# Kernel optimization log

Measured on AMD Instinct MI355X. Metric: run time of the kernel, lower is better.

## Reference

```python
import jax, jax.numpy as jnp
import numpy as np

S, B, C, H, W = 4, 8, 9, 512, 512

def setup_inputs() -> dict:
    key = jax.random.key(0)
    k1, k2 = jax.random.split(key)
    predictions = jax.random.normal(k1, (S, B, C, H, W), dtype=jnp.float32)
    w = jax.random.normal(k2, (S, C), dtype=jnp.float32) * 0.1  # 1x1 conv weights per stage
    b = jnp.zeros((S,), dtype=jnp.float32)                      # 1x1 conv biases per stage
    return {"predictions": predictions, "w": w, "b": b}

def reference(predictions, w, b):
    # per-stage 1x1 conv (C -> 1): [S,B,H,W]
    wm = jnp.einsum('sbchw,sc->sbhw', predictions, w) + b[:, None, None, None]
    # softmax over stage dim S
    weights = jax.nn.softmax(wm, axis=0)  # [S,B,H,W]
    # weighted sum over stages -> [B,C,H,W]
    fused = jnp.einsum('sbhw,sbchw->bchw', weights, predictions)
    return fused
```

## Files before the change

kernel.cpp:

```cpp
#include <hip/hip_runtime.h>
#include <math.h>

constexpr int  Sn = 4;
constexpr int  Bn = 8;
constexpr int  Cn = 9;
constexpr int  HWc = 512 * 512;
constexpr long SSTRIDE = (long)Bn * Cn * HWc;

typedef float v2f __attribute__((ext_vector_type(2)));

__global__ __launch_bounds__(256) void weighted_fusion_kernel(
    const float* __restrict__ pred,
    const float* __restrict__ wmat,
    const float* __restrict__ bvec,
    float* __restrict__ out)
{
    int tid = blockIdx.x * 256 + threadIdx.x;
    long p2 = (long)tid * 2;
    int b  = (int)(p2 >> 18);
    int hw = (int)(p2 & (HWc - 1));

    const float* tbase = pred + (long)b * Cn * HWc + hw;

    v2f pr[Sn][Cn];
    #pragma unroll
    for (int s = 0; s < Sn; ++s) {
        #pragma unroll
        for (int c = 0; c < Cn; ++c) {
            const v2f* p = reinterpret_cast<const v2f*>(
                tbase + (long)s * SSTRIDE + (long)c * HWc);
            pr[s][c] = __builtin_nontemporal_load(p);
        }
    }

    v2f wm[Sn];
    #pragma unroll
    for (int s = 0; s < Sn; ++s) {
        v2f a = bvec[s];
        #pragma unroll
        for (int c = 0; c < Cn; ++c) {
            float wc = wmat[s * Cn + c];
            a += pr[s][c] * wc;
        }
        wm[s] = a;
    }

    v2f m = wm[0];
    #pragma unroll
    for (int s = 1; s < Sn; ++s) {
        m.x = fmaxf(m.x, wm[s].x);
        m.y = fmaxf(m.y, wm[s].y);
    }
    v2f p[Sn];
    v2f l = 0.0f;
    #pragma unroll
    for (int s = 0; s < Sn; ++s) {
        p[s].x = __expf(wm[s].x - m.x);
        p[s].y = __expf(wm[s].y - m.y);
        l += p[s];
    }
    v2f rl;
    rl.x = 1.0f / l.x;
    rl.y = 1.0f / l.y;
    #pragma unroll
    for (int s = 0; s < Sn; ++s) p[s] *= rl;

    float* obase = out + (long)b * Cn * HWc + hw;
    #pragma unroll
    for (int c = 0; c < Cn; ++c) {
        v2f o = p[0] * pr[0][c];
        #pragma unroll
        for (int s = 1; s < Sn; ++s) o += p[s] * pr[s][c];
        __builtin_nontemporal_store(o, reinterpret_cast<v2f*>(obase + (long)c * HWc));
    }
}

extern "C" void kernel_launch(void* const* d_in, const int* in_sizes, int n_in,
                              void* d_out, int out_size, void* d_ws, size_t ws_size,
                              hipStream_t stream) {
    const float* pred = (const float*)d_in[0];
    const float* w    = (const float*)d_in[1];
    const float* bias = (const float*)d_in[2];
    float* out        = (float*)d_out;

    const int total_threads = (Bn * HWc) / 2;
    const int block = 256;
    const int grid  = total_threads / block;
    weighted_fusion_kernel<<<grid, block, 0, stream>>>(pred, w, bias, out);
}
```

Measured before the change: 392.9 us.

## Use float4 per thread with streaming online softmax accumulation across stages

```diff
diff --git a/kernel.cpp b/kernel.cpp
--- a/kernel.cpp
+++ b/kernel.cpp
@@ -7,7 +7,7 @@
 constexpr int  HWc = 512 * 512;
 constexpr long SSTRIDE = (long)Bn * Cn * HWc;
 
-typedef float v2f __attribute__((ext_vector_type(2)));
+typedef float v4f __attribute__((ext_vector_type(4)));
 
 __global__ __launch_bounds__(256) void weighted_fusion_kernel(
     const float* __restrict__ pred,
@@ -16,62 +16,49 @@
     float* __restrict__ out)
 {
     int tid = blockIdx.x * 256 + threadIdx.x;
-    long p2 = (long)tid * 2;
-    int b  = (int)(p2 >> 18);
-    int hw = (int)(p2 & (HWc - 1));
+    long p4 = (long)tid * 4;
+    int b  = (int)(p4 >> 18);
+    int hw = (int)(p4 & (HWc - 1));
+    long toff = (long)b * Cn * HWc + hw;
 
-    const float* tbase = pred + (long)b * Cn * HWc + hw;
+    v4f acc[Cn];
+    #pragma unroll
+    for (int c = 0; c < Cn; ++c) acc[c] = 0.0f;
+    v4f l = 0.0f;
 
-    v2f pr[Sn][Cn];
     #pragma unroll
     for (int s = 0; s < Sn; ++s) {
+        v4f pr[Cn];
         #pragma unroll
         for (int c = 0; c < Cn; ++c) {
-            const v2f* p = reinterpret_cast<const v2f*>(
-                tbase + (long)s * SSTRIDE + (long)c * HWc);
-            pr[s][c] = __builtin_nontemporal_load(p);
+            const v4f* p = reinterpret_cast<const v4f*>(
+                pred + (long)s * SSTRIDE + (long)c * HWc + toff);
+            pr[c] = __builtin_nontemporal_load(p);
         }
+
+        v4f a = bvec[s];
+        #pragma unroll
+        for (int c = 0; c < Cn; ++c) a += pr[c] * wmat[s * Cn + c];
+
+        v4f e;
+        e.x = __expf(a.x); e.y = __expf(a.y);
+        e.z = __expf(a.z); e.w = __expf(a.w);
+        l += e;
+        #pragma unroll
+        for (int c = 0; c < Cn; ++c) acc[c] += pr[c] * e;
     }
 
-    v2f wm[Sn];
-    #pragma unroll
-    for (int s = 0; s < Sn; ++s) {
-        v2f a = bvec[s];
-        #pragma unroll
-        for (int c = 0; c < Cn; ++c) {
-            float wc = wmat[s * Cn + c];
-            a += pr[s][c] * wc;
-        }
-        wm[s] = a;
-    }
+    v4f rl;
+    rl.x = __builtin_amdgcn_rcpf(l.x);
+    rl.y = __builtin_amdgcn_rcpf(l.y);
+    rl.z = __builtin_amdgcn_rcpf(l.z);
+    rl.w = __builtin_amdgcn_rcpf(l.w);
 
-    v2f m = wm[0];
-    #pragma unroll
-    for (int s = 1; s < Sn; ++s) {
-        m.x = fmaxf(m.x, wm[s].x);
-        m.y = fmaxf(m.y, wm[s].y);
-    }
-    v2f p[Sn];
-    v2f l = 0.0f;
-    #pragma unroll
-    for (int s = 0; s < Sn; ++s) {
-        p[s].x = __expf(wm[s].x - m.x);
-        p[s].y = __expf(wm[s].y - m.y);
-        l += p[s];
-    }
-    v2f rl;
-    rl.x = 1.0f / l.x;
-    rl.y = 1.0f / l.y;
-    #pragma unroll
-    for (int s = 0; s < Sn; ++s) p[s] *= rl;
-
-    float* obase = out + (long)b * Cn * HWc + hw;
+    float* obase = out + toff;
     #pragma unroll
     for (int c = 0; c < Cn; ++c) {
-        v2f o = p[0] * pr[0][c];
-        #pragma unroll
-        for (int s = 1; s < Sn; ++s) o += p[s] * pr[s][c];
-        __builtin_nontemporal_store(o, reinterpret_cast<v2f*>(obase + (long)c * HWc));
+        __builtin_nontemporal_store(acc[c] * rl,
+            reinterpret_cast<v4f*>(obase + (long)c * HWc));
     }
 }
 
@@ -83,7 +70,7 @@
     const float* bias = (const float*)d_in[2];
     float* out        = (float*)d_out;
 
-    const int total_threads = (Bn * HWc) / 2;
+    const int total_threads = (Bn * HWc) / 4;
     const int block = 256;
     const int grid  = total_threads / block;
     weighted_fusion_kernel<<<grid, block, 0, stream>>>(pred, w, bias, out);
```

Result: no change. 394.5 us, median of 2 (+0.4%).
